# Performance work log

Measured on AMD Instinct MI355X. Metric: run time of the kernel, lower is better.

The kernel has to match this reference:

```python
import jax, jax.numpy as jnp
import numpy as np

N, D_IN, D_OUT, K = 8192, 64, 128, 16


def setup_inputs() -> dict:
    key = jax.random.key(0)
    k1, k2, k3 = jax.random.split(key, 3)
    x = jax.random.normal(k1, (N, D_IN), dtype=jnp.float32)
    W1 = jax.random.normal(k2, (2 * D_IN, D_OUT), dtype=jnp.float32) * 0.05
    b1 = jnp.zeros((D_OUT,), dtype=jnp.float32)
    W2 = jax.random.normal(k3, (D_OUT, D_OUT), dtype=jnp.float32) * 0.05
    b2 = jnp.zeros((D_OUT,), dtype=jnp.float32)
    return {"x": x, "W1": W1, "b1": b1, "W2": W2, "b2": b2, "k": K}


def reference(x, W1, b1, W2, b2, k):
    # dynamic kNN graph (PyG knn(x, x, k) includes self as nearest neighbor)
    sq = jnp.sum(x * x, axis=-1)                      # [N]
    dist = sq[:, None] + sq[None, :] - 2.0 * (x @ x.T)  # [N, N] squared dists
    _, idx = jax.lax.top_k(-dist, k)                  # [N, k] nearest indices
    x_j = x[idx]                                      # [N, k, D_IN] gather
    x_i = jnp.broadcast_to(x[:, None, :], x_j.shape)  # [N, k, D_IN]
    e = jnp.concatenate([x_i, x_j - x_i], axis=-1)    # [N, k, 2*D_IN]
    h = jax.nn.relu(e @ W1 + b1) @ W2 + b2            # [N, k, D_OUT]
    return jnp.mean(h, axis=1)                        # mean aggregation -> [N, D_OUT]
```

## Files before the change

kernel.cpp:

```cpp
#include <hip/hip_runtime.h>

#define N 8192
#define DIN 64
#define DOUT 128
#define KNN 16
#define MSAMP 2048
#define NBX 16
#define NST 8
#define CAND_R 64
#define CAND_C (NBX * CAND_R)
#define EPS 1.0f
#define DELTA_Q 64
#define VCAP 128
#define ROWS_PRE 16

typedef unsigned long long u64;
typedef __attribute__((ext_vector_type(8))) short bf16x8;
typedef __attribute__((ext_vector_type(4))) float floatx4;

__device__ __forceinline__ unsigned mono(float f) {
    unsigned u = __float_as_uint(f);
    return (u & 0x80000000u) ? ~u : (u | 0x80000000u);
}
__device__ __forceinline__ unsigned short f2bf(float f) {
    unsigned u = __float_as_uint(f);
    return (unsigned short)((u + 0x7FFFu + ((u >> 16) & 1u)) >> 16);
}
__device__ __forceinline__ unsigned qdist(float dist) {
    int q = (int)(dist * 128.0f) + 2;
    q = max(q, 0); return (unsigned)min(q, 65535);
}

__global__ __launch_bounds__(256) void k_pre(const float* __restrict__ x,
                                             const float* __restrict__ W1,
                                             const float* __restrict__ b1,
                                             float* __restrict__ sq,
                                             float* __restrict__ sqs,
                                             unsigned short* __restrict__ Xh,
                                             float* __restrict__ U,
                                             float* __restrict__ V) {
    __shared__ float xs[ROWS_PRE][DIN];
    int t = threadIdx.x;
    int r0 = blockIdx.x * ROWS_PRE;
    float4 xv = ((const float4*)x)[(size_t)r0 * (DIN / 4) + t];
    ((float4*)xs)[t] = xv;
    ushort4 h4;
    h4.x = f2bf(xv.x); h4.y = f2bf(xv.y);
    h4.z = f2bf(xv.z); h4.w = f2bf(xv.w);
    *(ushort4*)&Xh[r0 * DIN + t * 4] = h4;
    __syncthreads();
    if (t < ROWS_PRE) {
        const float4* xr = (const float4*)xs[t];
        float s0 = 0.f, s1 = 0.f, s2 = 0.f, s3 = 0.f;
#pragma unroll
        for (int q = 0; q < DIN / 4; ++q) {
            float4 a = xr[q];
            s0 = fmaf(a.x, a.x, s0); s1 = fmaf(a.y, a.y, s1);
            s2 = fmaf(a.z, a.z, s2); s3 = fmaf(a.w, a.w, s3);
        }
        float sv = (s0 + s1) + (s2 + s3);
        sq[r0 + t] = sv;
        if ((t & 3) == 0) sqs[(r0 + t) >> 2] = sv;
    }
    int o = t & 127, g = t >> 7;
    float aU[8], aV[8];
#pragma unroll
    for (int u = 0; u < 8; ++u) { aU[u] = 0.f; aV[u] = 0.f; }
    for (int kk = 0; kk < DIN; ++kk) {
        float whi = W1[kk * DOUT + o];
        float wlo = W1[(DIN + kk) * DOUT + o];
        float wd = whi - wlo;
#pragma unroll
        for (int u = 0; u < 8; ++u) {
            float xvv = xs[g * 8 + u][kk];
            aU[u] = fmaf(xvv, wd, aU[u]);
            aV[u] = fmaf(xvv, wlo, aV[u]);
        }
    }
    float bb = b1[o];
#pragma unroll
    for (int u = 0; u < 8; ++u) {
        int r = r0 + g * 8 + u;
        U[(size_t)r * DOUT + o] = aU[u] + bb;
        V[(size_t)r * DOUT + o] = aV[u];
    }
}

__global__ __launch_bounds__(512, 4) void k_pretau(const unsigned short* __restrict__ Xh,
                                                   const float* __restrict__ sq,
                                                   const float* __restrict__ sqs,
                                                   float* __restrict__ tauf) {
    __shared__ __align__(16) unsigned short qls[16 * MSAMP];
    int tid = threadIdx.x, w = tid >> 6, l = tid & 63;
    int m = l & 15, quad = l >> 4, ko = quad * 8;
    int rt = blockIdx.x;
    int irow = rt * 16 + m;
    size_t arow = (size_t)irow * DIN;
    bf16x8 iH0 = *(const bf16x8*)(Xh + arow + ko);
    bf16x8 iH1 = *(const bf16x8*)(Xh + arow + 32 + ko);
    float si = sq[irow];
    int swz = (m & 7) << 4;
    for (int it = 0; it < 16; ++it) {
        int s16 = w * 256 + it * 16;
        size_t srowA = (size_t)(4 * (s16 + m)) * DIN;
        bf16x8 sH0 = *(const bf16x8*)(Xh + srowA + ko);
        bf16x8 sH1 = *(const bf16x8*)(Xh + srowA + 32 + ko);
        floatx4 acc = {0.f, 0.f, 0.f, 0.f};
        acc = __builtin_amdgcn_mfma_f32_16x16x32_bf16(sH0, iH0, acc, 0, 0, 0);
        acc = __builtin_amdgcn_mfma_f32_16x16x32_bf16(sH1, iH1, acc, 0, 0, 0);
        int sc0 = s16 + quad * 4;
        float4 sj = *(const float4*)(sqs + sc0);
        unsigned q0 = qdist(fmaf(-2.0f, acc[0], si + sj.x));
        unsigned q1 = qdist(fmaf(-2.0f, acc[1], si + sj.y));
        unsigned q2 = qdist(fmaf(-2.0f, acc[2], si + sj.z));
        unsigned q3 = qdist(fmaf(-2.0f, acc[3], si + sj.w));
        u64 pk = (u64)q0 | ((u64)q1 << 16) | ((u64)q2 << 32) | ((u64)q3 << 48);
        *(u64*)&qls[m * MSAMP + (sc0 ^ swz)] = pk;
    }
    __syncthreads();
#pragma unroll
    for (int rr = 0; rr < 2; ++rr) {
        int rsub = w * 2 + rr;
        unsigned v[MSAMP / 64];
#pragma unroll
        for (int u = 0; u < MSAMP / 64; ++u)
            v[u] = qls[rsub * MSAMP + l + 64 * u];
        unsigned p = 0;
#pragma unroll
        for (int b = 15; b >= 0; --b) {
            unsigned c16 = p | (1u << b);
            int cnt = 0;
#pragma unroll
            for (int u = 0; u < MSAMP / 64; ++u)
                cnt += __popcll(__ballot(v[u] < c16));
            if (cnt < 16) p = c16;
        }
        if (l == 0) tauf[rt * 16 + rsub] = (float)p * (1.0f / 128.0f);
    }
}

__global__ __launch_bounds__(256, 8) void k_main(const unsigned short* __restrict__ Xh,
                                                 const float* __restrict__ sq,
                                                 const float* __restrict__ tauf,
                                                 unsigned* __restrict__ cand,
                                                 unsigned* __restrict__ cntpart) {
    __shared__ __align__(16) short ldsH[64 * 72];
    int tid = threadIdx.x, w = tid >> 6, l = tid & 63;
    int m = l & 15, ko = (l >> 4) * 8;
    int bx = blockIdx.x;
    int rt = blockIdx.y * 4 + w;
    size_t arow = (size_t)(rt * 16 + m) * DIN;
    bf16x8 aH0 = *(const bf16x8*)(Xh + arow + ko);
    bf16x8 aH1 = *(const bf16x8*)(Xh + arow + 32 + ko);
    int rg[4]; float T[4]; float si[4]; int rowcnt[4];
#pragma unroll
    for (int reg = 0; reg < 4; ++reg) {
        rg[reg] = rt * 16 + (l >> 4) * 4 + reg;
        si[reg] = sq[rg[reg]];
        T[reg] = tauf[rg[reg]] + EPS - si[reg];
        rowcnt[reg] = 0;
    }
    int qs = l & 48;
    unsigned lmask = (1u << (l & 15)) - 1u;
    int srw = tid >> 3, scol8 = (tid & 7) * 8;

    for (int st = 0; st < NST; ++st) {
        int jbase = bx * (NST * 64) + st * 64;
        __syncthreads();
        *(bf16x8*)&ldsH[srw * 72 + scol8] =
            *(const bf16x8*)(Xh + (size_t)(jbase + srw) * DIN + scol8);
        *(bf16x8*)&ldsH[(srw + 32) * 72 + scol8] =
            *(const bf16x8*)(Xh + (size_t)(jbase + srw + 32) * DIN + scol8);
        __syncthreads();
#pragma unroll
        for (int it = 0; it < 4; ++it) {
            int br = it * 16 + m;
            bf16x8 bH0 = *(const bf16x8*)&ldsH[br * 72 + ko];
            bf16x8 bH1 = *(const bf16x8*)&ldsH[br * 72 + 32 + ko];
            floatx4 acc = {0.f, 0.f, 0.f, 0.f};
            acc = __builtin_amdgcn_mfma_f32_16x16x32_bf16(aH0, bH0, acc, 0, 0, 0);
            acc = __builtin_amdgcn_mfma_f32_16x16x32_bf16(aH1, bH1, acc, 0, 0, 0);
            int jcol = jbase + it * 16 + m;
            float sqj = sq[jcol];
#pragma unroll
            for (int reg = 0; reg < 4; ++reg) {
                float tv = fmaf(-2.0f, acc[reg], sqj);
                bool pass = tv <= T[reg];
                u64 bal = __ballot(pass);
                if (bal) {
                    unsigned m16 = (unsigned)((bal >> qs) & 0xFFFFull);
                    if (pass) {
                        int slot = rowcnt[reg] + __popc(m16 & lmask);
                        if (slot < CAND_R)
                            cand[(size_t)rg[reg] * CAND_C + bx * CAND_R + slot] =
                                (qdist(tv + si[reg]) << 16) | (unsigned)jcol;
                    }
                    rowcnt[reg] += __popc(m16);
                }
            }
        }
    }
    if ((l & 15) == 0) {
#pragma unroll
        for (int reg = 0; reg < 4; ++reg)
            cntpart[rg[reg] * NBX + bx] = (unsigned)min(rowcnt[reg], CAND_R);
    }
}

__global__ __launch_bounds__(256, 8) void k_post(
    const float* __restrict__ x, const float* __restrict__ sq,
    const unsigned* __restrict__ cntpart, const unsigned* __restrict__ cand,
    const float* __restrict__ U, const float* __restrict__ V,
    const float* __restrict__ W2, const float* __restrict__ b2,
    float* __restrict__ out)
{
    __shared__ union {
        struct { unsigned short vlist[4][VCAP];
                 u64 ekeys[4][VCAP]; } e;
        struct { float ag[4][DOUT];
                 float w2t[32 * DOUT]; } a;
    } sm;
    __shared__ int knn_s[4][KNN];
    int t = threadIdx.x;
    int w = t >> 6, l = t & 63;
    int row = blockIdx.x * 4 + w;
    {
        unsigned c[NBX];
        const unsigned* cp = cntpart + (size_t)row * NBX;
#pragma unroll
        for (int b = 0; b < NBX; ++b) c[b] = min(cp[b], (unsigned)CAND_R);
        const unsigned* crow = cand + (size_t)row * CAND_C;
        unsigned qq[NBX];
#pragma unroll
        for (int u = 0; u < NBX; ++u) {
            unsigned kv = crow[u * 64 + l];
            qq[u] = ((unsigned)l < c[u]) ? (kv >> 16) : 0xFFFFFFFFu;
        }
        unsigned p = 0;
#pragma unroll
        for (int b = 15; b >= 0; --b) {
            unsigned c16 = p | (1u << b);
            int cnt = 0;
#pragma unroll
            for (int u = 0; u < NBX; ++u)
                cnt += __popcll(__ballot(qq[u] < c16));
            if (cnt < 16) p = c16;
        }
        unsigned thr = p + DELTA_Q;
        int nv = 0;
        u64 lm = (l == 63) ? 0xFFFFFFFFFFFFFFFFull >> 1 : (1ull << l) - 1ull;
#pragma unroll
        for (int u = 0; u < NBX; ++u) {
            bool pred = qq[u] <= thr;
            u64 bal = __ballot(pred);
            int slot = nv + __popcll(bal & lm);
            if (pred && slot < VCAP) {
                unsigned kv = crow[u * 64 + l];
                sm.e.vlist[w][slot] = (unsigned short)(kv & 0xFFFFu);
            }
            nv += __popcll(bal);
        }
        nv = min(nv, VCAP);
        __syncthreads();
        float sqi = sq[row];
        const float* xi = x + (size_t)row * DIN;
#pragma unroll
        for (int r = 0; r < VCAP / 64; ++r) {
            int v = l + 64 * r;
            if (v < nv) {
                int j = (int)sm.e.vlist[w][v];
                const float4* bj = (const float4*)(x + (size_t)j * DIN);
                float s0 = 0.f, s1 = 0.f, s2 = 0.f, s3 = 0.f;
                float4 rb[8];
#pragma unroll
                for (int q = 0; q < 8; ++q) rb[q] = bj[q];
#pragma unroll
                for (int q = 0; q < 8; ++q) {
                    s0 = fmaf(xi[4 * q + 0], rb[q].x, s0);
                    s1 = fmaf(xi[4 * q + 1], rb[q].y, s1);
                    s2 = fmaf(xi[4 * q + 2], rb[q].z, s2);
                    s3 = fmaf(xi[4 * q + 3], rb[q].w, s3);
                }
#pragma unroll
                for (int q = 0; q < 8; ++q) rb[q] = bj[8 + q];
#pragma unroll
                for (int q = 0; q < 8; ++q) {
                    s0 = fmaf(xi[32 + 4 * q + 0], rb[q].x, s0);
                    s1 = fmaf(xi[32 + 4 * q + 1], rb[q].y, s1);
                    s2 = fmaf(xi[32 + 4 * q + 2], rb[q].z, s2);
                    s3 = fmaf(xi[32 + 4 * q + 3], rb[q].w, s3);
                }
                float d = (s0 + s1) + (s2 + s3);
                float dist = fmaf(-2.0f, d, sqi + sq[j]);
                sm.e.ekeys[w][v] = ((u64)mono(dist) << 32) | (unsigned)j;
            }
        }
#pragma unroll
        for (int r = 0; r < VCAP / 64; ++r) {
            int v = l + 64 * r;
            if (v < nv) {
                u64 mykey = sm.e.ekeys[w][v];
                int rank = 0;
                for (int i = 0; i < nv; ++i)
                    rank += (sm.e.ekeys[w][i] < mykey) ? 1 : 0;
                if (rank < KNN)
                    knn_s[w][rank] = (int)(unsigned)(mykey & 0xFFFFFFFFull);
            }
        }
    }
    __syncthreads();
    {
        int o = t & 127, g = t >> 7;
        int row0 = blockIdx.x * 4;
#pragma unroll
        for (int r = 0; r < 2; ++r) {
            int rr = g * 2 + r;
            int i = row0 + rr;
            float u = U[(size_t)i * DOUT + o];
            float acc = 0.f;
#pragma unroll
            for (int q = 0; q < KNN; ++q)
                acc += fmaxf(u + V[(size_t)knn_s[rr][q] * DOUT + o], 0.0f);
            sm.a.ag[rr][o] = acc * (1.0f / KNN);
        }
        float a2[2] = {0.f, 0.f};
#pragma unroll
        for (int tile = 0; tile < 4; ++tile) {
            __syncthreads();
#pragma unroll
            for (int u = 0; u < 4; ++u)
                ((float4*)sm.a.w2t)[t + u * 256] =
                    ((const float4*)(W2 + tile * 32 * DOUT))[t + u * 256];
            __syncthreads();
#pragma unroll 8
            for (int kk = 0; kk < 32; ++kk) {
                float wv = sm.a.w2t[kk * DOUT + o];
#pragma unroll
                for (int r = 0; r < 2; ++r)
                    a2[r] = fmaf(sm.a.ag[g * 2 + r][tile * 32 + kk], wv, a2[r]);
            }
        }
        float bb = b2[o];
#pragma unroll
        for (int r = 0; r < 2; ++r)
            out[(size_t)(row0 + g * 2 + r) * DOUT + o] = a2[r] + bb;
    }
}

extern "C" void kernel_launch(void* const* d_in, const int* in_sizes, int n_in,
                              void* d_out, int out_size, void* d_ws, size_t ws_size,
                              hipStream_t stream) {
    const float* x  = (const float*)d_in[0];
    const float* W1 = (const float*)d_in[1];
    const float* b1 = (const float*)d_in[2];
    const float* W2 = (const float*)d_in[3];
    const float* b2 = (const float*)d_in[4];
    float* out = (float*)d_out;

    char* ws = (char*)d_ws;
    float*          sq      = (float*)(ws);
    float*          sqs     = (float*)(ws + 32768);
    float*          tauf    = (float*)(ws + 40960);
    unsigned short* Xh      = (unsigned short*)(ws + 655360);
    float*          U       = (float*)(ws + 2097152);
    float*          V       = (float*)(ws + 6291456);
    unsigned*       cntpart = (unsigned*)(ws + 10485760);
    unsigned*       cand    = (unsigned*)(ws + 11534336);

    k_pre<<<N / ROWS_PRE, 256, 0, stream>>>(x, W1, b1, sq, sqs, Xh, U, V);
    k_pretau<<<N / 16, 512, 0, stream>>>(Xh, sq, sqs, tauf);
    k_main<<<dim3(NBX, 128), 256, 0, stream>>>(Xh, sq, tauf, cand, cntpart);
    k_post<<<N / 4, 256, 0, stream>>>(x, sq, cntpart, cand, U, V, W2, b2, out);
}
```

Measured before the change: 171.7 us.

## Shrink pre-pass blocks and compact sample rows for tau estimation

k_pre now processes 4 rows per block instead of 16 and also writes a compact bf16 copy of every 4th row (the sample set) into a separate buffer. k_pretau then reads the sample rows contiguously from this buffer instead of striding through Xh. It also handles 8 query rows per block with half the LDS, and each wave now computes tau for a single row. The aim is more blocks and better occupancy in both small kernels plus cheaper sample loads. The cost is that half of each MFMA tile's output is discarded and W1 is reloaded by more blocks.

```diff
diff --git a/kernel.cpp b/kernel.cpp
--- a/kernel.cpp
+++ b/kernel.cpp
@@ -12,7 +12,6 @@
 #define EPS 1.0f
 #define DELTA_Q 64
 #define VCAP 128
-#define ROWS_PRE 16
 
 typedef unsigned long long u64;
 typedef __attribute__((ext_vector_type(8))) short bf16x8;
@@ -31,25 +30,30 @@
     q = max(q, 0); return (unsigned)min(q, 65535);
 }
 
-__global__ __launch_bounds__(256) void k_pre(const float* __restrict__ x,
-                                             const float* __restrict__ W1,
-                                             const float* __restrict__ b1,
-                                             float* __restrict__ sq,
-                                             float* __restrict__ sqs,
-                                             unsigned short* __restrict__ Xh,
-                                             float* __restrict__ U,
-                                             float* __restrict__ V) {
-    __shared__ float xs[ROWS_PRE][DIN];
+__global__ __launch_bounds__(256, 8) void k_pre(const float* __restrict__ x,
+                                                const float* __restrict__ W1,
+                                                const float* __restrict__ b1,
+                                                float* __restrict__ sq,
+                                                float* __restrict__ sqs,
+                                                unsigned short* __restrict__ Xh,
+                                                unsigned short* __restrict__ Xs,
+                                                float* __restrict__ U,
+                                                float* __restrict__ V) {
+    __shared__ float xs[4][DIN];
     int t = threadIdx.x;
-    int r0 = blockIdx.x * ROWS_PRE;
-    float4 xv = ((const float4*)x)[(size_t)r0 * (DIN / 4) + t];
-    ((float4*)xs)[t] = xv;
-    ushort4 h4;
-    h4.x = f2bf(xv.x); h4.y = f2bf(xv.y);
-    h4.z = f2bf(xv.z); h4.w = f2bf(xv.w);
-    *(ushort4*)&Xh[r0 * DIN + t * 4] = h4;
+    int r0 = blockIdx.x * 4;
+    if (t < 64) {
+        float4 xv = ((const float4*)x)[(size_t)r0 * (DIN / 4) + t];
+        ((float4*)xs)[t] = xv;
+        ushort4 h4;
+        h4.x = f2bf(xv.x); h4.y = f2bf(xv.y);
+        h4.z = f2bf(xv.z); h4.w = f2bf(xv.w);
+        *(ushort4*)&Xh[r0 * DIN + t * 4] = h4;
+        if (t < 16)
+            *(ushort4*)&Xs[(r0 >> 2) * DIN + t * 4] = h4;
+    }
     __syncthreads();
-    if (t < ROWS_PRE) {
+    if (t < 4) {
         const float4* xr = (const float4*)xs[t];
         float s0 = 0.f, s1 = 0.f, s2 = 0.f, s3 = 0.f;
 #pragma unroll
@@ -60,41 +64,42 @@
         }
         float sv = (s0 + s1) + (s2 + s3);
         sq[r0 + t] = sv;
-        if ((t & 3) == 0) sqs[(r0 + t) >> 2] = sv;
+        if (t == 0) sqs[r0 >> 2] = sv;
     }
     int o = t & 127, g = t >> 7;
-    float aU[8], aV[8];
-#pragma unroll
-    for (int u = 0; u < 8; ++u) { aU[u] = 0.f; aV[u] = 0.f; }
+    float aU[2], aV[2];
+#pragma unroll
+    for (int u = 0; u < 2; ++u) { aU[u] = 0.f; aV[u] = 0.f; }
     for (int kk = 0; kk < DIN; ++kk) {
         float whi = W1[kk * DOUT + o];
         float wlo = W1[(DIN + kk) * DOUT + o];
         float wd = whi - wlo;
 #pragma unroll
-        for (int u = 0; u < 8; ++u) {
-            float xvv = xs[g * 8 + u][kk];
+        for (int u = 0; u < 2; ++u) {
+            float xvv = xs[g * 2 + u][kk];
             aU[u] = fmaf(xvv, wd, aU[u]);
             aV[u] = fmaf(xvv, wlo, aV[u]);
         }
     }
     float bb = b1[o];
 #pragma unroll
-    for (int u = 0; u < 8; ++u) {
-        int r = r0 + g * 8 + u;
+    for (int u = 0; u < 2; ++u) {
+        int r = r0 + g * 2 + u;
         U[(size_t)r * DOUT + o] = aU[u] + bb;
         V[(size_t)r * DOUT + o] = aV[u];
     }
 }
 
-__global__ __launch_bounds__(512, 4) void k_pretau(const unsigned short* __restrict__ Xh,
+__global__ __launch_bounds__(512, 6) void k_pretau(const unsigned short* __restrict__ Xh,
+                                                   const unsigned short* __restrict__ Xs,
                                                    const float* __restrict__ sq,
                                                    const float* __restrict__ sqs,
                                                    float* __restrict__ tauf) {
-    __shared__ __align__(16) unsigned short qls[16 * MSAMP];
+    __shared__ __align__(16) unsigned short qls[8 * MSAMP];
     int tid = threadIdx.x, w = tid >> 6, l = tid & 63;
     int m = l & 15, quad = l >> 4, ko = quad * 8;
     int rt = blockIdx.x;
-    int irow = rt * 16 + m;
+    int irow = rt * 8 + (m & 7);
     size_t arow = (size_t)irow * DIN;
     bf16x8 iH0 = *(const bf16x8*)(Xh + arow + ko);
     bf16x8 iH1 = *(const bf16x8*)(Xh + arow + 32 + ko);
@@ -102,9 +107,9 @@
     int swz = (m & 7) << 4;
     for (int it = 0; it < 16; ++it) {
         int s16 = w * 256 + it * 16;
-        size_t srowA = (size_t)(4 * (s16 + m)) * DIN;
-        bf16x8 sH0 = *(const bf16x8*)(Xh + srowA + ko);
-        bf16x8 sH1 = *(const bf16x8*)(Xh + srowA + 32 + ko);
+        const unsigned short* sp = Xs + (size_t)(s16 + m) * DIN;
+        bf16x8 sH0 = *(const bf16x8*)(sp + ko);
+        bf16x8 sH1 = *(const bf16x8*)(sp + 32 + ko);
         floatx4 acc = {0.f, 0.f, 0.f, 0.f};
         acc = __builtin_amdgcn_mfma_f32_16x16x32_bf16(sH0, iH0, acc, 0, 0, 0);
         acc = __builtin_amdgcn_mfma_f32_16x16x32_bf16(sH1, iH1, acc, 0, 0, 0);
@@ -114,29 +119,27 @@
         unsigned q1 = qdist(fmaf(-2.0f, acc[1], si + sj.y));
         unsigned q2 = qdist(fmaf(-2.0f, acc[2], si + sj.z));
         unsigned q3 = qdist(fmaf(-2.0f, acc[3], si + sj.w));
-        u64 pk = (u64)q0 | ((u64)q1 << 16) | ((u64)q2 << 32) | ((u64)q3 << 48);
-        *(u64*)&qls[m * MSAMP + (sc0 ^ swz)] = pk;
+        if (m < 8) {
+            u64 pk = (u64)q0 | ((u64)q1 << 16) | ((u64)q2 << 32) | ((u64)q3 << 48);
+            *(u64*)&qls[m * MSAMP + (sc0 ^ swz)] = pk;
+        }
     }
     __syncthreads();
-#pragma unroll
-    for (int rr = 0; rr < 2; ++rr) {
-        int rsub = w * 2 + rr;
-        unsigned v[MSAMP / 64];
+    unsigned v[MSAMP / 64];
+#pragma unroll
+    for (int u = 0; u < MSAMP / 64; ++u)
+        v[u] = qls[w * MSAMP + l + 64 * u];
+    unsigned p = 0;
+#pragma unroll
+    for (int b = 15; b >= 0; --b) {
+        unsigned c16 = p | (1u << b);
+        int cnt = 0;
 #pragma unroll
         for (int u = 0; u < MSAMP / 64; ++u)
-            v[u] = qls[rsub * MSAMP + l + 64 * u];
-        unsigned p = 0;
-#pragma unroll
-        for (int b = 15; b >= 0; --b) {
-            unsigned c16 = p | (1u << b);
-            int cnt = 0;
-#pragma unroll
-            for (int u = 0; u < MSAMP / 64; ++u)
-                cnt += __popcll(__ballot(v[u] < c16));
-            if (cnt < 16) p = c16;
-        }
-        if (l == 0) tauf[rt * 16 + rsub] = (float)p * (1.0f / 128.0f);
-    }
+            cnt += __popcll(__ballot(v[u] < c16));
+        if (cnt < 16) p = c16;
+    }
+    if (l == 0) tauf[rt * 8 + w] = (float)p * (1.0f / 128.0f);
 }
 
 __global__ __launch_bounds__(256, 8) void k_main(const unsigned short* __restrict__ Xh,
@@ -361,14 +364,15 @@
     float*          sq      = (float*)(ws);
     float*          sqs     = (float*)(ws + 32768);
     float*          tauf    = (float*)(ws + 40960);
+    unsigned short* Xs      = (unsigned short*)(ws + 73728);
     unsigned short* Xh      = (unsigned short*)(ws + 655360);
     float*          U       = (float*)(ws + 2097152);
     float*          V       = (float*)(ws + 6291456);
     unsigned*       cntpart = (unsigned*)(ws + 10485760);
     unsigned*       cand    = (unsigned*)(ws + 11534336);
 
-    k_pre<<<N / ROWS_PRE, 256, 0, stream>>>(x, W1, b1, sq, sqs, Xh, U, V);
-    k_pretau<<<N / 16, 512, 0, stream>>>(Xh, sq, sqs, tauf);
+    k_pre<<<N / 4, 256, 0, stream>>>(x, W1, b1, sq, sqs, Xh, Xs, U, V);
+    k_pretau<<<N / 8, 512, 0, stream>>>(Xh, Xs, sq, sqs, tauf);
     k_main<<<dim3(NBX, 128), 256, 0, stream>>>(Xh, sq, tauf, cand, cntpart);
     k_post<<<N / 4, 256, 0, stream>>>(x, sq, cntpart, cand, U, V, W2, b2, out);
 }
```

New measurement: 192.1 us. 11.8% more time.
